# Kernel optimization log

Measured on AMD Instinct MI355X. Metric: run time of the kernel, lower is better.

The kernel has to match this reference:

```python
import jax, jax.numpy as jnp
import numpy as np

R = 6
P = 2 * R + 1          # 13, correlation patch size
N = P * P              # 169 displacements
C = 32                 # one-hot label channels
FOUR_LN2 = 4.0 * float(np.log(2.0))


def _extract_windows(x, h, w):
    """Zero-pad by R and extract all PxP shifted views.
    x: (b, c, h, w) -> (b, c, N, h, w), displacement index n = dy*P + dx,
    matching both SpatialCorrelationSampler patch ordering and F.unfold."""
    xp = jnp.pad(x, ((0, 0), (0, 0), (R, R), (R, R)))
    return jnp.stack([xp[:, :, dy:dy + h, dx:dx + w]
                      for dy in range(P) for dx in range(P)], axis=2)


def setup_inputs():
    key = jax.random.key(0)
    k1, k2, k3 = jax.random.split(key, 3)
    feats_r = jax.random.normal(k1, (2, 2, 128, 64, 64), dtype=jnp.float32)
    feats_t = jax.random.normal(k2, (2, 128, 64, 64), dtype=jnp.float32)
    quantized_r = jax.random.randint(k3, (2, 2, 1, 256, 256), 0, C)
    return {"feats_r": feats_r, "feats_t": feats_t, "quantized_r": quantized_r}


def reference(feats_r, feats_t, quantized_r):
    nref, b, c, h, w = feats_r.shape
    hw = h * w

    # ---- local PxP correlation volume per reference (SpatialCorrelationSampler, k=1) ----
    corrs = []
    for i in range(nref):
        win = _extract_windows(feats_r[i], h, w)                       # (b,c,N,h,w)
        corrs.append(jnp.einsum('bchw,bcnhw->bnhw', feats_t, win).reshape(b, N, hw))
    corr = jax.nn.softmax(jnp.concatenate(corrs, axis=1), axis=1)      # (b, nref*N, hw)

    # ---- compact_verify: top-2 + gaussian heatmap refinement ----
    cc = corr.reshape(b, nref, N, hw).transpose(0, 1, 3, 2).reshape(b, nref * hw, N)
    ccd = jax.lax.stop_gradient(cc)                                     # torch uses .detach()
    vals, idx = jax.lax.top_k(ccd, 2)                                   # (b, L, 2)
    wts = jax.nn.softmax(vals, axis=-1)
    ys = (idx // P).astype(jnp.float32)
    xs = (idx % P).astype(jnp.float32)
    grid = jnp.arange(P, dtype=jnp.float32)
    dx = grid[None, None, None, :] - xs[..., None]                      # (b,L,2,P)
    dy = grid[None, None, None, :] - ys[..., None]                      # (b,L,2,P)
    heat = jnp.exp(-FOUR_LN2 * (dx[:, :, :, None, :] ** 2 + dy[:, :, :, :, None] ** 2))  # (b,L,2,P,P) [yy,xx]
    corr_heat = jnp.einsum('blkn,blk->bln', heat.reshape(b, nref * hw, 2, N), wts)
    vmax = jnp.max(vals, axis=-1, keepdims=True)
    corr2 = jnp.where(vmax > 0.1, corr_heat, cc)                        # mask/refine
    corr2 = corr2.reshape(b, nref, hw, N).transpose(0, 1, 3, 2).reshape(b, nref * N, hw)

    # ---- get_out: unfold one-hot reference labels and weighted-sum over window ----
    scale = quantized_r.shape[-2] // h                                  # prep: stride subsample
    ufs = []
    for i in range(nref):
        lab = quantized_r[i, :, 0, ::scale, ::scale]                    # (b,h,w)
        oh = jnp.transpose(jax.nn.one_hot(lab, C, dtype=feats_t.dtype), (0, 3, 1, 2))
        ufs.append(_extract_windows(oh, h, w).reshape(b, C, N, hw))
    image_uf = jnp.concatenate(ufs, axis=2)                             # (b,C,nref*N,hw)
    image_uf = image_uf.at[:, 1:].multiply(1.15)                        # inference boost
    out = jnp.einsum('bnl,bcnl->bcl', corr2, image_uf)
    return out.reshape(b, C, h, w)
```

## Files before the change

### kernel.cpp

```cpp
#include <hip/hip_runtime.h>
#include <math.h>

namespace {

constexpr int RAD  = 6;
constexpr int P    = 13;
constexpr int NWIN = 169;
constexpr int NTOT = 338;
constexpr int NCH  = 128;
constexpr int NCLS = 32;
constexpr int W    = 64;
constexpr int HW   = 4096;
constexpr float FOUR_LN2 = 2.772588722239781f;

constexpr int TX    = 32;
constexpr int CHUNK = 8;
constexpr int PW    = 48;
constexpr int PR    = 13;
constexpr int FRELEMS = CHUNK * PR * PW;
constexpr int NCHUNK  = NCH / CHUNK;
constexpr int TILE    = TX * NWIN;

__device__ __forceinline__ bool better(float va, int ia, float vb, int ib) {
  return (va > vb) || ((va == vb) && (ia < ib));
}

__global__ __launch_bounds__(256, 2) void corr_kernel(
    const float* __restrict__ fr,
    const float* __restrict__ ft,
    float* __restrict__ vol) {
  const int blk = blockIdx.x;
  const int xh = blk & 1;
  const int y  = (blk >> 1) & 63;
  const int bi = blk >> 7;
  const int b  = bi >> 1;
  const int ii = bi & 1;
  const int x0 = xh * TX;
  const int t  = threadIdx.x;
  const int cg = t >> 7;
  const int tl = t & 127;

  __shared__ __align__(16) float smem[2 * FRELEMS];
  __shared__ __align__(16) float ftbuf[2][CHUNK * TX];

  const int xg = tl & 7;
  const int dy = tl >> 3;
  const bool comp = (tl < 104);

  const float* frbase = fr + (size_t)((ii * 2 + b) * NCH) * HW;
  const float* ftp = ft + (size_t)(b * NCH + (t >> 5)) * HW + y * W + x0 + (t & 31);

  int offc[20];
  unsigned vmsk = 0u;
  #pragma unroll
  for (int u = 0; u < 20; ++u) {
    const int e = t + u * 256;
    int o = 0;
    if (e < FRELEMS) {
      const int cc  = e / (PR * PW);
      const int rem = e - cc * (PR * PW);
      const int r   = rem / PW;
      const int xc  = rem - r * PW;
      const int yy  = y + r - RAD;
      const int xx  = x0 - RAD + xc;
      if ((unsigned)yy < 64u && (unsigned)xx < 64u && xc < 44) {
        o = cc * HW + yy * W + xx;
        vmsk |= (1u << u);
      }
    }
    offc[u] = o;
  }

  float acc[13][4];
  #pragma unroll
  for (int dx = 0; dx < 13; ++dx)
    #pragma unroll
    for (int k = 0; k < 4; ++k) acc[dx][k] = 0.f;

  float rg[20];
  float rft;

  auto stage_load = [&](int c0) {
    const float* fb = frbase + (size_t)c0 * HW;
    #pragma unroll
    for (int u = 0; u < 20; ++u) {
      const float v = fb[offc[u]];
      rg[u] = (vmsk & (1u << u)) ? v : 0.f;
    }
    rft = ftp[(size_t)c0 * HW];
  };
  auto stage_write = [&](int s) {
    float* frb = smem + s * FRELEMS;
    #pragma unroll
    for (int u = 0; u < 20; ++u) {
      const int e = t + u * 256;
      if (e < FRELEMS) frb[e] = rg[u];
    }
    ftbuf[s][t] = rft;
  };

  stage_load(0);
  stage_write(0);
  __syncthreads();

  for (int k = 0; k < NCHUNK; ++k) {
    const int cur = k & 1;
    if (k < NCHUNK - 1) stage_load((k + 1) * CHUNK);
    if (comp) {
      const float* frb = smem + cur * FRELEMS;
      #pragma unroll
      for (int c2 = 0; c2 < 4; ++c2) {
        const int cc = cg * 4 + c2;
        const float* fp = frb + (cc * PR + dy) * PW + xg * 4;
        float w[16];
        #pragma unroll
        for (int j = 0; j < 4; ++j) {
          const float4 q4 = *(const float4*)(fp + 4 * j);
          w[4 * j] = q4.x; w[4 * j + 1] = q4.y; w[4 * j + 2] = q4.z; w[4 * j + 3] = q4.w;
        }
        const float4 tq = *(const float4*)(&ftbuf[cur][cc * TX + xg * 4]);
        const float tqa[4] = {tq.x, tq.y, tq.z, tq.w};
        #pragma unroll
        for (int dx = 0; dx < 13; ++dx)
          #pragma unroll
          for (int kk = 0; kk < 4; ++kk)
            acc[dx][kk] = fmaf(w[dx + kk], tqa[kk], acc[dx][kk]);
      }
    }
    __syncthreads();
    if (k < NCHUNK - 1) stage_write(cur ^ 1);
    __syncthreads();
  }

  if (comp && cg == 1) {
    float* rb = smem + tl * 52;
    #pragma unroll
    for (int dx = 0; dx < 13; ++dx)
      *(float4*)(rb + dx * 4) = make_float4(acc[dx][0], acc[dx][1], acc[dx][2], acc[dx][3]);
  }
  __syncthreads();
  if (comp && cg == 0) {
    const float* rb = smem + tl * 52;
    #pragma unroll
    for (int dx = 0; dx < 13; ++dx) {
      const float4 r = *(const float4*)(rb + dx * 4);
      acc[dx][0] += r.x; acc[dx][1] += r.y; acc[dx][2] += r.z; acc[dx][3] += r.w;
    }
  }
  __syncthreads();
  if (comp && cg == 0) {
    #pragma unroll
    for (int dx = 0; dx < 13; ++dx)
      #pragma unroll
      for (int kk = 0; kk < 4; ++kk)
        smem[(xg * 4 + kk) * NWIN + dy * 13 + dx] = acc[dx][kk];
  }
  __syncthreads();
  {
    float* gb = vol + ((size_t)(b * HW + y * W + x0) * 2 + ii) * NWIN;
    for (int u = 0; u < 22; ++u) {
      const int e = t + u * 256;
      if (e < TILE) {
        const int xl2 = e / NWIN;
        const int mm  = e - xl2 * NWIN;
        gb[(size_t)xl2 * (2 * NWIN) + mm] = smem[e];
      }
    }
  }
}

__global__ __launch_bounds__(256) void lab_kernel(
    const int* __restrict__ q, int* __restrict__ lab) {
  const int idx = blockIdx.x * 256 + threadIdx.x;
  const int i2b = idx >> 12;
  const int rem = idx & 4095;
  const int yy  = rem >> 6;
  const int xx  = rem & 63;
  lab[idx] = q[(size_t)i2b * 65536 + (yy * 4) * 256 + xx * 4];
}

__global__ __launch_bounds__(256) void post_kernel(
    const float* __restrict__ vol,
    const int*  __restrict__ lab,
    float* __restrict__ out) {
  const int blk  = blockIdx.x;
  const int t    = threadIdx.x;
  const int w    = t >> 6;
  const int lane = t & 63;
  const int pix  = blk * 4 + w;
  const int b = pix >> 12;
  const int y = (pix >> 6) & 63;
  const int x = pix & 63;

  __shared__ float accS[4][NCLS];
  accS[w][lane & 31] = 0.f;

  float vv[6];
  float lmax = -INFINITY;
  const float* vp = vol + (size_t)pix * NTOT;
  #pragma unroll
  for (int k = 0; k < 6; ++k) {
    const int e = lane + 64 * k;
    vv[k] = (e < NTOT) ? vp[e] : -INFINITY;
    lmax = fmaxf(lmax, vv[k]);
  }
  #pragma unroll
  for (int off = 32; off > 0; off >>= 1)
    lmax = fmaxf(lmax, __shfl_xor(lmax, off));

  float p[6];
  float lsum = 0.f;
  #pragma unroll
  for (int k = 0; k < 6; ++k) {
    const int e = lane + 64 * k;
    p[k] = (e < NTOT) ? __expf(vv[k] - lmax) : 0.f;
    lsum += p[k];
  }
  #pragma unroll
  for (int off = 32; off > 0; off >>= 1)
    lsum += __shfl_xor(lsum, off);
  const float rinv = 1.f / lsum;
  #pragma unroll
  for (int k = 0; k < 6; ++k) p[k] *= rinv;

  float a1_0 = -1.f, a2_0 = -1.f, a1_1 = -1.f, a2_1 = -1.f;
  int   j1_0 = 1 << 20, j2_0 = 1 << 20, j1_1 = 1 << 20, j2_1 = 1 << 20;
  #pragma unroll
  for (int k = 0; k < 6; ++k) {
    const int e = lane + 64 * k;
    if (e < NTOT) {
      const int r = (e >= NWIN) ? 1 : 0;
      const int m = e - r * NWIN;
      const float pv = p[k];
      if (r == 0) {
        if (better(pv, m, a1_0, j1_0)) { a2_0 = a1_0; j2_0 = j1_0; a1_0 = pv; j1_0 = m; }
        else if (better(pv, m, a2_0, j2_0)) { a2_0 = pv; j2_0 = m; }
      } else {
        if (better(pv, m, a1_1, j1_1)) { a2_1 = a1_1; j2_1 = j1_1; a1_1 = pv; j1_1 = m; }
        else if (better(pv, m, a2_1, j2_1)) { a2_1 = pv; j2_1 = m; }
      }
    }
  }
  #pragma unroll
  for (int off = 32; off > 0; off >>= 1) {
    {
      const float u1 = __shfl_xor(a1_0, off); const int q1 = __shfl_xor(j1_0, off);
      const float u2 = __shfl_xor(a2_0, off); const int q2 = __shfl_xor(j2_0, off);
      if (better(u1, q1, a1_0, j1_0)) {
        float nv2; int ni2;
        if (better(a1_0, j1_0, u2, q2)) { nv2 = a1_0; ni2 = j1_0; }
        else                            { nv2 = u2;   ni2 = q2; }
        a1_0 = u1; j1_0 = q1; a2_0 = nv2; j2_0 = ni2;
      } else if (better(u1, q1, a2_0, j2_0)) { a2_0 = u1; j2_0 = q1; }
    }
    {
      const float u1 = __shfl_xor(a1_1, off); const int q1 = __shfl_xor(j1_1, off);
      const float u2 = __shfl_xor(a2_1, off); const int q2 = __shfl_xor(j2_1, off);
      if (better(u1, q1, a1_1, j1_1)) {
        float nv2; int ni2;
        if (better(a1_1, j1_1, u2, q2)) { nv2 = a1_1; ni2 = j1_1; }
        else                            { nv2 = u2;   ni2 = q2; }
        a1_1 = u1; j1_1 = q1; a2_1 = nv2; j2_1 = ni2;
      } else if (better(u1, q1, a2_1, j2_1)) { a2_1 = u1; j2_1 = q1; }
    }
  }

  const float e10 = __expf(a1_0), e20 = __expf(a2_0);
  const float rs0 = 1.f / (e10 + e20);
  const float w00 = e10 * rs0, w10 = e20 * rs0;
  const bool  fl0 = (a1_0 > 0.1f);
  const float xs00 = (float)(j1_0 % P), ys00 = (float)(j1_0 / P);
  const float xs10 = (float)(j2_0 % P), ys10 = (float)(j2_0 / P);

  const float e11 = __expf(a1_1), e21 = __expf(a2_1);
  const float rs1 = 1.f / (e11 + e21);
  const float w01 = e11 * rs1, w11 = e21 * rs1;
  const bool  fl1 = (a1_1 > 0.1f);
  const float xs01 = (float)(j1_1 % P), ys01 = (float)(j1_1 / P);
  const float xs11 = (float)(j2_1 % P), ys11 = (float)(j2_1 / P);

  #pragma unroll
  for (int k = 0; k < 6; ++k) {
    const int e = lane + 64 * k;
    if (e < NTOT) {
      const int r  = (e >= NWIN) ? 1 : 0;
      const int m  = e - r * NWIN;
      const int dy = m / P;
      const int dx = m - dy * P;
      const bool  fl = r ? fl1 : fl0;
      float val;
      if (fl) {
        const float wA = r ? w01 : w00, wB = r ? w11 : w10;
        const float xA = r ? xs01 : xs00, yA = r ? ys01 : ys00;
        const float xB = r ? xs11 : xs10, yB = r ? ys11 : ys10;
        const float fdx0 = (float)dx - xA, fdy0 = (float)dy - yA;
        const float fdx1 = (float)dx - xB, fdy1 = (float)dy - yB;
        val = wA * __expf(-FOUR_LN2 * (fdx0 * fdx0 + fdy0 * fdy0))
            + wB * __expf(-FOUR_LN2 * (fdx1 * fdx1 + fdy1 * fdy1));
      } else {
        val = p[k];
      }
      const int yy = y + dy - RAD;
      const int xx = x + dx - RAD;
      if ((unsigned)yy < 64u && (unsigned)xx < 64u) {
        const int cls = lab[(size_t)(r * 2 + b) * 4096 + yy * W + xx];
        atomicAdd(&accS[w][cls], val);
      }
    }
  }
  __syncthreads();

  if (t < 4 * NCLS) {
    const int cls = t >> 2;
    const int j   = t & 3;
    const int x0  = (blk * 4) & 63;
    const float sc = (cls == 0) ? 1.0f : 1.15f;
    out[(size_t)(b * NCLS + cls) * HW + y * W + x0 + j] = accS[j][cls] * sc;
  }
}

}

extern "C" void kernel_launch(void* const* d_in, const int* in_sizes, int n_in,
                              void* d_out, int out_size, void* d_ws, size_t ws_size,
                              hipStream_t stream) {
  const float* fr = (const float*)d_in[0];
  const float* ft = (const float*)d_in[1];
  const int*   q  = (const int*)d_in[2];
  float* out = (float*)d_out;
  float* vol = (float*)d_ws;
  int*   lab = (int*)((char*)d_ws + (size_t)2 * HW * NTOT * sizeof(float));

  lab_kernel<<<dim3(64), dim3(256), 0, stream>>>(q, lab);
  corr_kernel<<<dim3(2 * 2 * 64 * 2), dim3(256), 0, stream>>>(fr, ft, vol);
  post_kernel<<<dim3(2 * HW / 4), dim3(256), 0, stream>>>(vol, lab, out);
}
```

Measured before the change: 60.88 us.

## Fuse correlation and softmax/top-k/label aggregation into one kernel

Merges the correlation kernel and the post-processing kernel into a single 512-thread block. Each block computes both reference volumes, one per half of the threads, and keeps the 32x338 correlation tile in shared memory. It then runs the softmax, top-2, heatmap and label accumulation directly from that tile. This removes the global write and re-read of the full correlation volume and one kernel launch. It also drops one barrier per chunk iteration. In exchange the grid shrinks to 256 larger blocks with higher LDS use, which lowers occupancy, and each wave now processes four pixels in sequence.

```diff
diff --git a/kernel.cpp b/kernel.cpp
--- a/kernel.cpp
+++ b/kernel.cpp
@@ -18,43 +18,56 @@
 constexpr int PW    = 48;
 constexpr int PR    = 13;
 constexpr int FRELEMS = CHUNK * PR * PW;
-constexpr int NCHUNK  = NCH / CHUNK;
-constexpr int TILE    = TX * NWIN;
+constexpr int NLD   = 20;
+constexpr int NCHUNK = NCH / CHUNK;
 
 __device__ __forceinline__ bool better(float va, int ia, float vb, int ib) {
   return (va > vb) || ((va == vb) && (ia < ib));
 }
 
-__global__ __launch_bounds__(256, 2) void corr_kernel(
+__global__ __launch_bounds__(256) void lab_kernel(
+    const int* __restrict__ q, int* __restrict__ lab) {
+  const int idx = blockIdx.x * 256 + threadIdx.x;
+  const int i2b = idx >> 12;
+  const int rem = idx & 4095;
+  const int yy  = rem >> 6;
+  const int xx  = rem & 63;
+  lab[idx] = q[(size_t)i2b * 65536 + (yy * 4) * 256 + xx * 4];
+}
+
+__global__ __launch_bounds__(512, 2) void fused_kernel(
     const float* __restrict__ fr,
     const float* __restrict__ ft,
-    float* __restrict__ vol) {
+    const int*  __restrict__ lab,
+    float* __restrict__ out) {
   const int blk = blockIdx.x;
   const int xh = blk & 1;
   const int y  = (blk >> 1) & 63;
-  const int bi = blk >> 7;
-  const int b  = bi >> 1;
-  const int ii = bi & 1;
+  const int b  = blk >> 7;
   const int x0 = xh * TX;
   const int t  = threadIdx.x;
-  const int cg = t >> 7;
-  const int tl = t & 127;
-
-  __shared__ __align__(16) float smem[2 * FRELEMS];
+  const int ii = t >> 8;
+  const int tt = t & 255;
+  const int cg = tt >> 7;
+  const int tl = tt & 127;
+
+  __shared__ __align__(16) float smem[4 * FRELEMS];
   __shared__ __align__(16) float ftbuf[2][CHUNK * TX];
+  __shared__ float accS[TX][NCLS];
 
   const int xg = tl & 7;
   const int dy = tl >> 3;
   const bool comp = (tl < 104);
 
+  float* stg = smem + ii * (2 * FRELEMS);
   const float* frbase = fr + (size_t)((ii * 2 + b) * NCH) * HW;
-  const float* ftp = ft + (size_t)(b * NCH + (t >> 5)) * HW + y * W + x0 + (t & 31);
-
-  int offc[20];
+  const float* ftp = ft + (size_t)(b * NCH + (tt >> 5)) * HW + y * W + x0 + (tt & 31);
+
+  int offc[NLD];
   unsigned vmsk = 0u;
   #pragma unroll
-  for (int u = 0; u < 20; ++u) {
-    const int e = t + u * 256;
+  for (int u = 0; u < NLD; ++u) {
+    const int e = tt + u * 256;
     int o = 0;
     if (e < FRELEMS) {
       const int cc  = e / (PR * PW);
@@ -77,26 +90,26 @@
     #pragma unroll
     for (int k = 0; k < 4; ++k) acc[dx][k] = 0.f;
 
-  float rg[20];
+  float rg[NLD];
   float rft;
 
   auto stage_load = [&](int c0) {
     const float* fb = frbase + (size_t)c0 * HW;
     #pragma unroll
-    for (int u = 0; u < 20; ++u) {
+    for (int u = 0; u < NLD; ++u) {
       const float v = fb[offc[u]];
       rg[u] = (vmsk & (1u << u)) ? v : 0.f;
     }
-    rft = ftp[(size_t)c0 * HW];
+    if (t < 256) rft = ftp[(size_t)c0 * HW];
   };
   auto stage_write = [&](int s) {
-    float* frb = smem + s * FRELEMS;
-    #pragma unroll
-    for (int u = 0; u < 20; ++u) {
-      const int e = t + u * 256;
+    float* frb = stg + s * FRELEMS;
+    #pragma unroll
+    for (int u = 0; u < NLD; ++u) {
+      const int e = tt + u * 256;
       if (e < FRELEMS) frb[e] = rg[u];
     }
-    ftbuf[s][t] = rft;
+    if (t < 256) ftbuf[s][tt] = rft;
   };
 
   stage_load(0);
@@ -107,7 +120,7 @@
     const int cur = k & 1;
     if (k < NCHUNK - 1) stage_load((k + 1) * CHUNK);
     if (comp) {
-      const float* frb = smem + cur * FRELEMS;
+      const float* frb = stg + cur * FRELEMS;
       #pragma unroll
       for (int c2 = 0; c2 < 4; ++c2) {
         const int cc = cg * 4 + c2;
@@ -127,195 +140,160 @@
             acc[dx][kk] = fmaf(w[dx + kk], tqa[kk], acc[dx][kk]);
       }
     }
-    __syncthreads();
     if (k < NCHUNK - 1) stage_write(cur ^ 1);
     __syncthreads();
   }
 
+  float* tile = smem;
   if (comp && cg == 1) {
-    float* rb = smem + tl * 52;
-    #pragma unroll
-    for (int dx = 0; dx < 13; ++dx)
-      *(float4*)(rb + dx * 4) = make_float4(acc[dx][0], acc[dx][1], acc[dx][2], acc[dx][3]);
-  }
-  __syncthreads();
-  if (comp && cg == 0) {
-    const float* rb = smem + tl * 52;
-    #pragma unroll
-    for (int dx = 0; dx < 13; ++dx) {
-      const float4 r = *(const float4*)(rb + dx * 4);
-      acc[dx][0] += r.x; acc[dx][1] += r.y; acc[dx][2] += r.z; acc[dx][3] += r.w;
-    }
-  }
-  __syncthreads();
-  if (comp && cg == 0) {
     #pragma unroll
     for (int dx = 0; dx < 13; ++dx)
       #pragma unroll
       for (int kk = 0; kk < 4; ++kk)
-        smem[(xg * 4 + kk) * NWIN + dy * 13 + dx] = acc[dx][kk];
-  }
+        tile[(xg * 4 + kk) * NTOT + ii * NWIN + dy * 13 + dx] = acc[dx][kk];
+  }
+  ((float*)accS)[t] = 0.f;
+  ((float*)accS)[t + 512] = 0.f;
   __syncthreads();
-  {
-    float* gb = vol + ((size_t)(b * HW + y * W + x0) * 2 + ii) * NWIN;
-    for (int u = 0; u < 22; ++u) {
-      const int e = t + u * 256;
-      if (e < TILE) {
-        const int xl2 = e / NWIN;
-        const int mm  = e - xl2 * NWIN;
-        gb[(size_t)xl2 * (2 * NWIN) + mm] = smem[e];
-      }
-    }
-  }
-}
-
-__global__ __launch_bounds__(256) void lab_kernel(
-    const int* __restrict__ q, int* __restrict__ lab) {
-  const int idx = blockIdx.x * 256 + threadIdx.x;
-  const int i2b = idx >> 12;
-  const int rem = idx & 4095;
-  const int yy  = rem >> 6;
-  const int xx  = rem & 63;
-  lab[idx] = q[(size_t)i2b * 65536 + (yy * 4) * 256 + xx * 4];
-}
-
-__global__ __launch_bounds__(256) void post_kernel(
-    const float* __restrict__ vol,
-    const int*  __restrict__ lab,
-    float* __restrict__ out) {
-  const int blk  = blockIdx.x;
-  const int t    = threadIdx.x;
-  const int w    = t >> 6;
+  if (comp && cg == 0) {
+    #pragma unroll
+    for (int dx = 0; dx < 13; ++dx)
+      #pragma unroll
+      for (int kk = 0; kk < 4; ++kk) {
+        const int idx = (xg * 4 + kk) * NTOT + ii * NWIN + dy * 13 + dx;
+        tile[idx] += acc[dx][kk];
+      }
+  }
+  __syncthreads();
+
+  const int wv   = t >> 6;
   const int lane = t & 63;
-  const int pix  = blk * 4 + w;
-  const int b = pix >> 12;
-  const int y = (pix >> 6) & 63;
-  const int x = pix & 63;
-
-  __shared__ float accS[4][NCLS];
-  accS[w][lane & 31] = 0.f;
-
-  float vv[6];
-  float lmax = -INFINITY;
-  const float* vp = vol + (size_t)pix * NTOT;
+  for (int j = 0; j < 4; ++j) {
+    const int px = (wv << 2) | j;
+    const int x  = x0 + px;
+    const float* tp = tile + (size_t)px * NTOT;
+
+    float vv[6];
+    float lmax = -INFINITY;
+    #pragma unroll
+    for (int k = 0; k < 6; ++k) {
+      const int e = lane + 64 * k;
+      vv[k] = (e < NTOT) ? tp[e] : -INFINITY;
+      lmax = fmaxf(lmax, vv[k]);
+    }
+    #pragma unroll
+    for (int off = 32; off > 0; off >>= 1)
+      lmax = fmaxf(lmax, __shfl_xor(lmax, off));
+
+    float p[6];
+    float lsum = 0.f;
+    #pragma unroll
+    for (int k = 0; k < 6; ++k) {
+      const int e = lane + 64 * k;
+      p[k] = (e < NTOT) ? __expf(vv[k] - lmax) : 0.f;
+      lsum += p[k];
+    }
+    #pragma unroll
+    for (int off = 32; off > 0; off >>= 1)
+      lsum += __shfl_xor(lsum, off);
+    const float rinv = 1.f / lsum;
+    #pragma unroll
+    for (int k = 0; k < 6; ++k) p[k] *= rinv;
+
+    float a1_0 = -1.f, a2_0 = -1.f, a1_1 = -1.f, a2_1 = -1.f;
+    int   j1_0 = 1 << 20, j2_0 = 1 << 20, j1_1 = 1 << 20, j2_1 = 1 << 20;
+    #pragma unroll
+    for (int k = 0; k < 6; ++k) {
+      const int e = lane + 64 * k;
+      if (e < NTOT) {
+        const int r = (e >= NWIN) ? 1 : 0;
+        const int m = e - r * NWIN;
+        const float pv = p[k];
+        if (r == 0) {
+          if (better(pv, m, a1_0, j1_0)) { a2_0 = a1_0; j2_0 = j1_0; a1_0 = pv; j1_0 = m; }
+          else if (better(pv, m, a2_0, j2_0)) { a2_0 = pv; j2_0 = m; }
+        } else {
+          if (better(pv, m, a1_1, j1_1)) { a2_1 = a1_1; j2_1 = j1_1; a1_1 = pv; j1_1 = m; }
+          else if (better(pv, m, a2_1, j2_1)) { a2_1 = pv; j2_1 = m; }
+        }
+      }
+    }
+    #pragma unroll
+    for (int off = 32; off > 0; off >>= 1) {
+      {
+        const float u1 = __shfl_xor(a1_0, off); const int q1 = __shfl_xor(j1_0, off);
+        const float u2 = __shfl_xor(a2_0, off); const int q2 = __shfl_xor(j2_0, off);
+        if (better(u1, q1, a1_0, j1_0)) {
+          float nv2; int ni2;
+          if (better(a1_0, j1_0, u2, q2)) { nv2 = a1_0; ni2 = j1_0; }
+          else                            { nv2 = u2;   ni2 = q2; }
+          a1_0 = u1; j1_0 = q1; a2_0 = nv2; j2_0 = ni2;
+        } else if (better(u1, q1, a2_0, j2_0)) { a2_0 = u1; j2_0 = q1; }
+      }
+      {
+        const float u1 = __shfl_xor(a1_1, off); const int q1 = __shfl_xor(j1_1, off);
+        const float u2 = __shfl_xor(a2_1, off); const int q2 = __shfl_xor(j2_1, off);
+        if (better(u1, q1, a1_1, j1_1)) {
+          float nv2; int ni2;
+          if (better(a1_1, j1_1, u2, q2)) { nv2 = a1_1; ni2 = j1_1; }
+          else                            { nv2 = u2;   ni2 = q2; }
+          a1_1 = u1; j1_1 = q1; a2_1 = nv2; j2_1 = ni2;
+        } else if (better(u1, q1, a2_1, j2_1)) { a2_1 = u1; j2_1 = q1; }
+      }
+    }
+
+    const float e10 = __expf(a1_0), e20 = __expf(a2_0);
+    const float rs0 = 1.f / (e10 + e20);
+    const float w00 = e10 * rs0, w10 = e20 * rs0;
+    const bool  fl0 = (a1_0 > 0.1f);
+    const float xs00 = (float)(j1_0 % P), ys00 = (float)(j1_0 / P);
+    const float xs10 = (float)(j2_0 % P), ys10 = (float)(j2_0 / P);
+
+    const float e11 = __expf(a1_1), e21 = __expf(a2_1);
+    const float rs1 = 1.f / (e11 + e21);
+    const float w01 = e11 * rs1, w11 = e21 * rs1;
+    const bool  fl1 = (a1_1 > 0.1f);
+    const float xs01 = (float)(j1_1 % P), ys01 = (float)(j1_1 / P);
+    const float xs11 = (float)(j2_1 % P), ys11 = (float)(j2_1 / P);
+
+    #pragma unroll
+    for (int k = 0; k < 6; ++k) {
+      const int e = lane + 64 * k;
+      if (e < NTOT) {
+        const int r   = (e >= NWIN) ? 1 : 0;
+        const int m   = e - r * NWIN;
+        const int dy2 = m / P;
+        const int dx2 = m - dy2 * P;
+        const bool fl = r ? fl1 : fl0;
+        float val;
+        if (fl) {
+          const float wA = r ? w01 : w00, wB = r ? w11 : w10;
+          const float xA = r ? xs01 : xs00, yA = r ? ys01 : ys00;
+          const float xB = r ? xs11 : xs10, yB = r ? ys11 : ys10;
+          const float fdx0 = (float)dx2 - xA, fdy0 = (float)dy2 - yA;
+          const float fdx1 = (float)dx2 - xB, fdy1 = (float)dy2 - yB;
+          val = wA * __expf(-FOUR_LN2 * (fdx0 * fdx0 + fdy0 * fdy0))
+              + wB * __expf(-FOUR_LN2 * (fdx1 * fdx1 + fdy1 * fdy1));
+        } else {
+          val = p[k];
+        }
+        const int yy = y + dy2 - RAD;
+        const int xx = x + dx2 - RAD;
+        if ((unsigned)yy < 64u && (unsigned)xx < 64u) {
+          const int cls = lab[(size_t)(r * 2 + b) * 4096 + yy * W + xx];
+          atomicAdd(&accS[px][cls], val);
+        }
+      }
+    }
+  }
+  __syncthreads();
+
   #pragma unroll
-  for (int k = 0; k < 6; ++k) {
-    const int e = lane + 64 * k;
-    vv[k] = (e < NTOT) ? vp[e] : -INFINITY;
-    lmax = fmaxf(lmax, vv[k]);
-  }
-  #pragma unroll
-  for (int off = 32; off > 0; off >>= 1)
-    lmax = fmaxf(lmax, __shfl_xor(lmax, off));
-
-  float p[6];
-  float lsum = 0.f;
-  #pragma unroll
-  for (int k = 0; k < 6; ++k) {
-    const int e = lane + 64 * k;
-    p[k] = (e < NTOT) ? __expf(vv[k] - lmax) : 0.f;
-    lsum += p[k];
-  }
-  #pragma unroll
-  for (int off = 32; off > 0; off >>= 1)
-    lsum += __shfl_xor(lsum, off);
-  const float rinv = 1.f / lsum;
-  #pragma unroll
-  for (int k = 0; k < 6; ++k) p[k] *= rinv;
-
-  float a1_0 = -1.f, a2_0 = -1.f, a1_1 = -1.f, a2_1 = -1.f;
-  int   j1_0 = 1 << 20, j2_0 = 1 << 20, j1_1 = 1 << 20, j2_1 = 1 << 20;
-  #pragma unroll
-  for (int k = 0; k < 6; ++k) {
-    const int e = lane + 64 * k;
-    if (e < NTOT) {
-      const int r = (e >= NWIN) ? 1 : 0;
-      const int m = e - r * NWIN;
-      const float pv = p[k];
-      if (r == 0) {
-        if (better(pv, m, a1_0, j1_0)) { a2_0 = a1_0; j2_0 = j1_0; a1_0 = pv; j1_0 = m; }
-        else if (better(pv, m, a2_0, j2_0)) { a2_0 = pv; j2_0 = m; }
-      } else {
-        if (better(pv, m, a1_1, j1_1)) { a2_1 = a1_1; j2_1 = j1_1; a1_1 = pv; j1_1 = m; }
-        else if (better(pv, m, a2_1, j2_1)) { a2_1 = pv; j2_1 = m; }
-      }
-    }
-  }
-  #pragma unroll
-  for (int off = 32; off > 0; off >>= 1) {
-    {
-      const float u1 = __shfl_xor(a1_0, off); const int q1 = __shfl_xor(j1_0, off);
-      const float u2 = __shfl_xor(a2_0, off); const int q2 = __shfl_xor(j2_0, off);
-      if (better(u1, q1, a1_0, j1_0)) {
-        float nv2; int ni2;
-        if (better(a1_0, j1_0, u2, q2)) { nv2 = a1_0; ni2 = j1_0; }
-        else                            { nv2 = u2;   ni2 = q2; }
-        a1_0 = u1; j1_0 = q1; a2_0 = nv2; j2_0 = ni2;
-      } else if (better(u1, q1, a2_0, j2_0)) { a2_0 = u1; j2_0 = q1; }
-    }
-    {
-      const float u1 = __shfl_xor(a1_1, off); const int q1 = __shfl_xor(j1_1, off);
-      const float u2 = __shfl_xor(a2_1, off); const int q2 = __shfl_xor(j2_1, off);
-      if (better(u1, q1, a1_1, j1_1)) {
-        float nv2; int ni2;
-        if (better(a1_1, j1_1, u2, q2)) { nv2 = a1_1; ni2 = j1_1; }
-        else                            { nv2 = u2;   ni2 = q2; }
-        a1_1 = u1; j1_1 = q1; a2_1 = nv2; j2_1 = ni2;
-      } else if (better(u1, q1, a2_1, j2_1)) { a2_1 = u1; j2_1 = q1; }
-    }
-  }
-
-  const float e10 = __expf(a1_0), e20 = __expf(a2_0);
-  const float rs0 = 1.f / (e10 + e20);
-  const float w00 = e10 * rs0, w10 = e20 * rs0;
-  const bool  fl0 = (a1_0 > 0.1f);
-  const float xs00 = (float)(j1_0 % P), ys00 = (float)(j1_0 / P);
-  const float xs10 = (float)(j2_0 % P), ys10 = (float)(j2_0 / P);
-
-  const float e11 = __expf(a1_1), e21 = __expf(a2_1);
-  const float rs1 = 1.f / (e11 + e21);
-  const float w01 = e11 * rs1, w11 = e21 * rs1;
-  const bool  fl1 = (a1_1 > 0.1f);
-  const float xs01 = (float)(j1_1 % P), ys01 = (float)(j1_1 / P);
-  const float xs11 = (float)(j2_1 % P), ys11 = (float)(j2_1 / P);
-
-  #pragma unroll
-  for (int k = 0; k < 6; ++k) {
-    const int e = lane + 64 * k;
-    if (e < NTOT) {
-      const int r  = (e >= NWIN) ? 1 : 0;
-      const int m  = e - r * NWIN;
-      const int dy = m / P;
-      const int dx = m - dy * P;
-      const bool  fl = r ? fl1 : fl0;
-      float val;
-      if (fl) {
-        const float wA = r ? w01 : w00, wB = r ? w11 : w10;
-        const float xA = r ? xs01 : xs00, yA = r ? ys01 : ys00;
-        const float xB = r ? xs11 : xs10, yB = r ? ys11 : ys10;
-        const float fdx0 = (float)dx - xA, fdy0 = (float)dy - yA;
-        const float fdx1 = (float)dx - xB, fdy1 = (float)dy - yB;
-        val = wA * __expf(-FOUR_LN2 * (fdx0 * fdx0 + fdy0 * fdy0))
-            + wB * __expf(-FOUR_LN2 * (fdx1 * fdx1 + fdy1 * fdy1));
-      } else {
-        val = p[k];
-      }
-      const int yy = y + dy - RAD;
-      const int xx = x + dx - RAD;
-      if ((unsigned)yy < 64u && (unsigned)xx < 64u) {
-        const int cls = lab[(size_t)(r * 2 + b) * 4096 + yy * W + xx];
-        atomicAdd(&accS[w][cls], val);
-      }
-    }
-  }
-  __syncthreads();
-
-  if (t < 4 * NCLS) {
-    const int cls = t >> 2;
-    const int j   = t & 3;
-    const int x0  = (blk * 4) & 63;
+  for (int o = t; o < TX * NCLS; o += 512) {
+    const int cls = o >> 5;
+    const int px  = o & 31;
     const float sc = (cls == 0) ? 1.0f : 1.15f;
-    out[(size_t)(b * NCLS + cls) * HW + y * W + x0 + j] = accS[j][cls] * sc;
+    out[(size_t)(b * NCLS + cls) * HW + y * W + x0 + px] = accS[px][cls] * sc;
   }
 }
 
@@ -328,10 +306,8 @@
   const float* ft = (const float*)d_in[1];
   const int*   q  = (const int*)d_in[2];
   float* out = (float*)d_out;
-  float* vol = (float*)d_ws;
-  int*   lab = (int*)((char*)d_ws + (size_t)2 * HW * NTOT * sizeof(float));
+  int*   lab = (int*)d_ws;
 
   lab_kernel<<<dim3(64), dim3(256), 0, stream>>>(q, lab);
-  corr_kernel<<<dim3(2 * 2 * 64 * 2), dim3(256), 0, stream>>>(fr, ft, vol);
-  post_kernel<<<dim3(2 * HW / 4), dim3(256), 0, stream>>>(vol, lab, out);
-}
+  fused_kernel<<<dim3(2 * 64 * 2), dim3(512), 0, stream>>>(fr, ft, lab, out);
+}
```

Result: slower. 63.15 us (+3.7%).

## Fuse label subsampling into corr kernel, swizzle blocks across XCDs, drop redundant barrier

Applied to the files above, without the earlier changes.

The label-subsampling kernel is folded into the first 64 blocks of the correlation kernel, removing one kernel launch and its serialization on the stream. Block indices are remapped so that consecutive hardware block IDs, which are spread round-robin over the XCDs, map to neighbouring logical tiles. This is meant to improve L2 reuse of the overlapping reference-feature rows within each XCD. One __syncthreads per channel chunk is removed; this relies on the double-buffered shared memory to keep the write into the other buffer race-free, and adds a small amount of label work to some correlation blocks.

```diff
diff --git a/kernel.cpp b/kernel.cpp
--- a/kernel.cpp
+++ b/kernel.cpp
@@ -18,8 +18,10 @@
 constexpr int PW    = 48;
 constexpr int PR    = 13;
 constexpr int FRELEMS = CHUNK * PR * PW;
-constexpr int NCHUNK  = NCH / CHUNK;
-constexpr int TILE    = TX * NWIN;
+constexpr int NLD   = 20;
+constexpr int NCHUNK = NCH / CHUNK;
+constexpr int TILE  = TX * NWIN;
+constexpr size_t VOLF = (size_t)2 * HW * NTOT;
 
 __device__ __forceinline__ bool better(float va, int ia, float vb, int ib) {
   return (va > vb) || ((va == vb) && (ia < ib));
@@ -28,15 +30,28 @@
 __global__ __launch_bounds__(256, 2) void corr_kernel(
     const float* __restrict__ fr,
     const float* __restrict__ ft,
-    float* __restrict__ vol) {
+    float* __restrict__ vol,
+    const int* __restrict__ q,
+    int* __restrict__ lab) {
   const int blk = blockIdx.x;
-  const int xh = blk & 1;
-  const int y  = (blk >> 1) & 63;
-  const int bi = blk >> 7;
+  const int t  = threadIdx.x;
+
+  if (blk < 64) {
+    const int idx = blk * 256 + t;
+    const int i2b = idx >> 12;
+    const int rem = idx & 4095;
+    const int y2  = rem >> 6;
+    const int x2  = rem & 63;
+    lab[idx] = q[(size_t)i2b * 65536 + (y2 * 4) * 256 + x2 * 4];
+  }
+
+  const int lb = (blk & 7) * 64 + (blk >> 3);
+  const int xh = lb & 1;
+  const int y  = (lb >> 1) & 63;
+  const int bi = lb >> 7;
   const int b  = bi >> 1;
   const int ii = bi & 1;
   const int x0 = xh * TX;
-  const int t  = threadIdx.x;
   const int cg = t >> 7;
   const int tl = t & 127;
 
@@ -50,10 +65,10 @@
   const float* frbase = fr + (size_t)((ii * 2 + b) * NCH) * HW;
   const float* ftp = ft + (size_t)(b * NCH + (t >> 5)) * HW + y * W + x0 + (t & 31);
 
-  int offc[20];
+  int offc[NLD];
   unsigned vmsk = 0u;
   #pragma unroll
-  for (int u = 0; u < 20; ++u) {
+  for (int u = 0; u < NLD; ++u) {
     const int e = t + u * 256;
     int o = 0;
     if (e < FRELEMS) {
@@ -77,13 +92,13 @@
     #pragma unroll
     for (int k = 0; k < 4; ++k) acc[dx][k] = 0.f;
 
-  float rg[20];
+  float rg[NLD];
   float rft;
 
   auto stage_load = [&](int c0) {
     const float* fb = frbase + (size_t)c0 * HW;
     #pragma unroll
-    for (int u = 0; u < 20; ++u) {
+    for (int u = 0; u < NLD; ++u) {
       const float v = fb[offc[u]];
       rg[u] = (vmsk & (1u << u)) ? v : 0.f;
     }
@@ -92,7 +107,7 @@
   auto stage_write = [&](int s) {
     float* frb = smem + s * FRELEMS;
     #pragma unroll
-    for (int u = 0; u < 20; ++u) {
+    for (int u = 0; u < NLD; ++u) {
       const int e = t + u * 256;
       if (e < FRELEMS) frb[e] = rg[u];
     }
@@ -127,7 +142,6 @@
             acc[dx][kk] = fmaf(w[dx + kk], tqa[kk], acc[dx][kk]);
       }
     }
-    __syncthreads();
     if (k < NCHUNK - 1) stage_write(cur ^ 1);
     __syncthreads();
   }
@@ -167,16 +181,6 @@
       }
     }
   }
-}
-
-__global__ __launch_bounds__(256) void lab_kernel(
-    const int* __restrict__ q, int* __restrict__ lab) {
-  const int idx = blockIdx.x * 256 + threadIdx.x;
-  const int i2b = idx >> 12;
-  const int rem = idx & 4095;
-  const int yy  = rem >> 6;
-  const int xx  = rem & 63;
-  lab[idx] = q[(size_t)i2b * 65536 + (yy * 4) * 256 + xx * 4];
 }
 
 __global__ __launch_bounds__(256) void post_kernel(
@@ -329,9 +333,8 @@
   const int*   q  = (const int*)d_in[2];
   float* out = (float*)d_out;
   float* vol = (float*)d_ws;
-  int*   lab = (int*)((char*)d_ws + (size_t)2 * HW * NTOT * sizeof(float));
-
-  lab_kernel<<<dim3(64), dim3(256), 0, stream>>>(q, lab);
-  corr_kernel<<<dim3(2 * 2 * 64 * 2), dim3(256), 0, stream>>>(fr, ft, vol);
+  int*   lab = (int*)((char*)d_ws + VOLF * sizeof(float));
+
+  corr_kernel<<<dim3(2 * 2 * 64 * 2), dim3(256), 0, stream>>>(fr, ft, vol, q, lab);
   post_kernel<<<dim3(2 * HW / 4), dim3(256), 0, stream>>>(vol, lab, out);
 }
```

Result: faster. 58.77 us, median of 2 (-3.5%).
